# Optimization experiments

Measured on AMD Instinct MI355X. Metric: run time of the kernel, lower is better.

## Reference

```python
import jax, jax.numpy as jnp
import numpy as np


def _pairwise_sqdist(x, y):
    # x: [B, N, D], y: [B, M, D] -> P: [B, N, M] squared euclidean distances
    xx = jnp.sum(x * x, axis=-1)              # [B, N]
    yy = jnp.sum(y * y, axis=-1)              # [B, M]
    zz = jnp.einsum('bnd,bmd->bnm', x, y)     # [B, N, M]
    return xx[:, :, None] + yy[:, None, :] - 2.0 * zz


def setup_inputs() -> dict:
    key = jax.random.key(0)
    k1, k2 = jax.random.split(key)
    B, N, D = 8, 8192, 3
    preds = jax.random.normal(k1, (B, N, D), dtype=jnp.float32)
    gts = jax.random.normal(k2, (B, N, D), dtype=jnp.float32)
    return {"preds": preds, "gts": gts}


def reference(preds, gts):
    # P = batch_pairwise_dist(gts, preds): P[b, i, j] = ||gts[b,i] - preds[b,j]||^2
    P = _pairwise_sqdist(gts, preds)          # [B, N_gts, N_preds]
    loss_1 = jnp.sum(jnp.min(P, axis=1))      # min over gts points
    loss_2 = jnp.sum(jnp.min(P, axis=2))      # min over pred points
    return loss_1 + loss_2
```

## Files before the change

kernel.cpp:

```cpp
#include <hip/hip_runtime.h>

typedef _Float16 f16;
typedef f16 half8 __attribute__((ext_vector_type(8)));
typedef float f32x16 __attribute__((ext_vector_type(16)));

#define BB 8
#define NN 8192
#define SETPTS (BB * NN)
#define NPTS (2 * SETPTS)
#define TQ NPTS

__device__ __forceinline__ void gload_lds16(const void* g, void* l) {
  __builtin_amdgcn_global_load_lds(
      (const __attribute__((address_space(1))) void*)g,
      (__attribute__((address_space(3))) void*)l, 16, 0, 0);
}

__global__ __launch_bounds__(256) void chamfer_prep(
    const float* __restrict__ preds, const float* __restrict__ gts,
    float* __restrict__ yy, half8* __restrict__ Aq, half8* __restrict__ Bq) {
  int idx = blockIdx.x * 256 + threadIdx.x;
  int s = idx >> 16;
  int off = idx & (SETPTS - 1);
  const float* src = s ? gts : preds;
  float x0 = src[off * 3 + 0], x1 = src[off * 3 + 1], x2 = src[off * 3 + 2];

  f16 h0 = (f16)x0; f16 l0 = (f16)(x0 - (float)h0);
  f16 h1 = (f16)x1; f16 l1 = (f16)(x1 - (float)h1);
  f16 h2 = (f16)x2; f16 l2 = (f16)(x2 - (float)h2);

  float Y0 = -2.f * x0, Y1 = -2.f * x1, Y2 = -2.f * x2;
  f16 H0 = (f16)Y0; f16 L0 = (f16)(Y0 - (float)H0);
  f16 H1 = (f16)Y1; f16 L1 = (f16)(Y1 - (float)H1);
  f16 H2 = (f16)Y2; f16 L2 = (f16)(Y2 - (float)H2);

  float yv = x0 * x0 + x1 * x1 + x2 * x2;
  f16 yh = (f16)yv; f16 yl = (f16)(yv - (float)yh);

  f16 one = (f16)1.f, zz = (f16)0.f;
  half8 A0 = {h0, l0, h0, l0, h1, l1, h1, l1};
  half8 A1 = {h2, l2, h2, l2, one, one, zz, zz};
  half8 B0 = {H0, H0, L0, L0, H1, H1, L1, L1};
  half8 B1 = {H2, H2, L2, L2, yh, yl, zz, zz};

  Aq[idx * 2 + 0] = A0; Aq[idx * 2 + 1] = A1;
  Bq[idx * 2 + 0] = B0; Bq[idx * 2 + 1] = B1;
  yy[idx] = yv;
}

template <int R>
__global__ __launch_bounds__(256, 4) void chamfer_mfma(
    const half8* __restrict__ Aq, const half8* __restrict__ Bq,
    float* __restrict__ partial) {
  constexpr int NSTEP = NN / R / 32;
  constexpr int CH = 16;
  constexpr int NCH = NSTEP / CH;
  __shared__ __align__(16) char lds[2][CH * 1024];

  int bi = blockIdx.x;
  int xcd = bi & 7;
  int idx = bi >> 3;
  int panel = xcd * 2 + (idx & 1);
  int dir = panel >> 3;
  int b = panel & 7;
  int sub = idx >> 1;
  int qb = sub & 31;
  int r = sub >> 5;

  int tid = threadIdx.x;
  int w = tid >> 6;
  int l = tid & 63;
  int l31 = l & 31;
  int lh = l >> 5;

  const half8* Qp =
      Aq + ((size_t)(dir * BB + b) * NN + qb * 256 + w * 64) * 2;
  half8 q0 = Qp[l31 * 2 + lh];
  half8 q1 = Qp[(32 + l31) * 2 + lh];

  const char* gpanel = (const char*)(Bq + ((size_t)((1 - dir) * BB + b) * NN +
                                           r * (NN / R)) * 2);
  int perm = ((l & 31) * 2 + (l >> 5)) * 16;

  auto stage = [&](int buf, int c) {
    const char* csrc = gpanel + (size_t)(c * CH + w * 4) * 1024 + perm;
    char* cdst = &lds[buf][w * 4 * 1024];
#pragma unroll
    for (int i = 0; i < 4; ++i)
      gload_lds16(csrc + i * 1024, cdst + i * 1024);
  };

  f32x16 zero;
#pragma unroll
  for (int i = 0; i < 16; ++i) zero[i] = 0.f;
  float run0 = 3.4e38f, run1 = 3.4e38f;

  stage(0, 0);
  __syncthreads();

#pragma unroll 1
  for (int ch = 0; ch < NCH; ++ch) {
    int par = ch & 1;
    if (ch + 1 < NCH) stage(par ^ 1, ch + 1);
    const half8* lb = (const half8*)&lds[par][0];
#pragma unroll 4
    for (int st = 0; st < CH; ++st) {
      half8 bt = lb[st * 64 + l];
      f32x16 oa = __builtin_amdgcn_mfma_f32_32x32x16_f16(bt, q0, zero, 0, 0, 0);
      f32x16 ob = __builtin_amdgcn_mfma_f32_32x32x16_f16(bt, q1, zero, 0, 0, 0);
      {
        float t0 = fminf(fminf(oa[0], oa[1]), oa[2]);
        float t1 = fminf(fminf(oa[3], oa[4]), oa[5]);
        float t2 = fminf(fminf(oa[6], oa[7]), oa[8]);
        float t3 = fminf(fminf(oa[9], oa[10]), oa[11]);
        float t4 = fminf(fminf(oa[12], oa[13]), oa[14]);
        float u0 = fminf(fminf(t0, t1), t2);
        float u1 = fminf(fminf(t3, t4), oa[15]);
        run0 = fminf(fminf(run0, u0), u1);
      }
      {
        float t0 = fminf(fminf(ob[0], ob[1]), ob[2]);
        float t1 = fminf(fminf(ob[3], ob[4]), ob[5]);
        float t2 = fminf(fminf(ob[6], ob[7]), ob[8]);
        float t3 = fminf(fminf(ob[9], ob[10]), ob[11]);
        float t4 = fminf(fminf(ob[12], ob[13]), ob[14]);
        float u0 = fminf(fminf(t0, t1), t2);
        float u1 = fminf(fminf(t3, t4), ob[15]);
        run1 = fminf(fminf(run1, u0), u1);
      }
    }
    __syncthreads();
  }

  float v0 = fminf(run0, __shfl_xor(run0, 32));
  float v1 = fminf(run1, __shfl_xor(run1, 32));

  size_t qflat = (size_t)(dir * BB + b) * NN + qb * 256 + w * 64;
  float* pr = partial + (size_t)r * TQ + qflat;
  if (lh == 0) {
    pr[l31] = v0;
    pr[32 + l31] = v1;
  }
}

template <int R>
__global__ __launch_bounds__(256) void chamfer_tail(
    const float* __restrict__ partial, const float* __restrict__ yy,
    float* __restrict__ out) {
  int q = blockIdx.x * 256 + threadIdx.x;
  float m = partial[q];
#pragma unroll
  for (int rr = 1; rr < R; ++rr) m = fminf(m, partial[(size_t)rr * TQ + q]);
  m += yy[q];
  __shared__ float s[256];
  s[threadIdx.x] = m;
  __syncthreads();
  for (int o = 128; o > 0; o >>= 1) {
    if (threadIdx.x < o) s[threadIdx.x] += s[threadIdx.x + o];
    __syncthreads();
  }
  if (threadIdx.x == 0) atomicAdd(out, s[0]);
}

extern "C" void kernel_launch(void* const* d_in, const int* in_sizes, int n_in,
                              void* d_out, int out_size, void* d_ws,
                              size_t ws_size, hipStream_t stream) {
  const float* preds = (const float*)d_in[0];
  const float* gts = (const float*)d_in[1];
  float* out = (float*)d_out;

  float* partial = (float*)d_ws;
  float* yy = partial + (size_t)2 * TQ;
  half8* Aq = (half8*)(yy + NPTS);
  half8* Bq = Aq + (size_t)NPTS * 2;

  hipMemsetAsync(out, 0, sizeof(float), stream);
  chamfer_prep<<<NPTS / 256, 256, 0, stream>>>(preds, gts, yy, Aq, Bq);
  chamfer_mfma<2><<<2 * BB * 32 * 2, 256, 0, stream>>>(Aq, Bq, partial);
  chamfer_tail<2><<<TQ / 256, 256, 0, stream>>>(partial, yy, out);
}
```

Before: 54.77 us.

## Drop reference-split, fuse yy add and block reduction into MFMA kernel

Each MFMA block now scans the full reference set (R=1) instead of half, so the cross-block min over partials disappears. The yy term is added and per-block sums are reduced inside the MFMA kernel. A single-block final kernel sums 512 block partials, which removes the memset, the atomic and the large partial buffer. The grid halves to 512 blocks, each doing twice the work, which may reduce parallelism and load balance across CUs.

New measurement: 47.22 us. 13.8% less time.

```diff
diff --git a/kernel.cpp b/kernel.cpp
--- a/kernel.cpp
+++ b/kernel.cpp
@@ -9,6 +9,7 @@
 #define SETPTS (BB * NN)
 #define NPTS (2 * SETPTS)
 #define TQ NPTS
+#define NBLK 512
 
 __device__ __forceinline__ void gload_lds16(const void* g, void* l) {
   __builtin_amdgcn_global_load_lds(
@@ -48,14 +49,14 @@
   yy[idx] = yv;
 }
 
-template <int R>
 __global__ __launch_bounds__(256, 4) void chamfer_mfma(
     const half8* __restrict__ Aq, const half8* __restrict__ Bq,
-    float* __restrict__ partial) {
-  constexpr int NSTEP = NN / R / 32;
+    const float* __restrict__ yy, float* __restrict__ bsums) {
+  constexpr int NSTEP = NN / 32;
   constexpr int CH = 16;
   constexpr int NCH = NSTEP / CH;
   __shared__ __align__(16) char lds[2][CH * 1024];
+  __shared__ float wsum[4];
 
   int bi = blockIdx.x;
   int xcd = bi & 7;
@@ -63,9 +64,7 @@
   int panel = xcd * 2 + (idx & 1);
   int dir = panel >> 3;
   int b = panel & 7;
-  int sub = idx >> 1;
-  int qb = sub & 31;
-  int r = sub >> 5;
+  int qb = idx >> 1;
 
   int tid = threadIdx.x;
   int w = tid >> 6;
@@ -73,13 +72,12 @@
   int l31 = l & 31;
   int lh = l >> 5;
 
-  const half8* Qp =
-      Aq + ((size_t)(dir * BB + b) * NN + qb * 256 + w * 64) * 2;
+  size_t qflat = (size_t)(dir * BB + b) * NN + qb * 256 + w * 64;
+  const half8* Qp = Aq + qflat * 2;
   half8 q0 = Qp[l31 * 2 + lh];
   half8 q1 = Qp[(32 + l31) * 2 + lh];
 
-  const char* gpanel = (const char*)(Bq + ((size_t)((1 - dir) * BB + b) * NN +
-                                           r * (NN / R)) * 2);
+  const char* gpanel = (const char*)(Bq + (size_t)((1 - dir) * BB + b) * NN * 2);
   int perm = ((l & 31) * 2 + (l >> 5)) * 16;
 
   auto stage = [&](int buf, int c) {
@@ -135,31 +133,33 @@
   float v0 = fminf(run0, __shfl_xor(run0, 32));
   float v1 = fminf(run1, __shfl_xor(run1, 32));
 
-  size_t qflat = (size_t)(dir * BB + b) * NN + qb * 256 + w * 64;
-  float* pr = partial + (size_t)r * TQ + qflat;
-  if (lh == 0) {
-    pr[l31] = v0;
-    pr[32 + l31] = v1;
-  }
+  float y0 = yy[qflat + l31];
+  float y1 = yy[qflat + 32 + l31];
+  float c = (v0 + y0) + (v1 + y1);
+  c += __shfl_xor(c, 1);
+  c += __shfl_xor(c, 2);
+  c += __shfl_xor(c, 4);
+  c += __shfl_xor(c, 8);
+  c += __shfl_xor(c, 16);
+  c *= 0.5f;
+  c *= 2.0f;
+  if (l == 0) wsum[w] = c;
+  __syncthreads();
+  if (tid == 0)
+    bsums[bi] = (wsum[0] + wsum[1]) + (wsum[2] + wsum[3]);
 }
 
-template <int R>
-__global__ __launch_bounds__(256) void chamfer_tail(
-    const float* __restrict__ partial, const float* __restrict__ yy,
-    float* __restrict__ out) {
-  int q = blockIdx.x * 256 + threadIdx.x;
-  float m = partial[q];
-#pragma unroll
-  for (int rr = 1; rr < R; ++rr) m = fminf(m, partial[(size_t)rr * TQ + q]);
-  m += yy[q];
+__global__ __launch_bounds__(256) void chamfer_final(
+    const float* __restrict__ bsums, float* __restrict__ out) {
+  float v = bsums[threadIdx.x] + bsums[threadIdx.x + 256];
   __shared__ float s[256];
-  s[threadIdx.x] = m;
+  s[threadIdx.x] = v;
   __syncthreads();
   for (int o = 128; o > 0; o >>= 1) {
     if (threadIdx.x < o) s[threadIdx.x] += s[threadIdx.x + o];
     __syncthreads();
   }
-  if (threadIdx.x == 0) atomicAdd(out, s[0]);
+  if (threadIdx.x == 0) out[0] = s[0];
 }
 
 extern "C" void kernel_launch(void* const* d_in, const int* in_sizes, int n_in,
@@ -169,13 +169,12 @@
   const float* gts = (const float*)d_in[1];
   float* out = (float*)d_out;
 
-  float* partial = (float*)d_ws;
-  float* yy = partial + (size_t)2 * TQ;
+  float* bsums = (float*)d_ws;
+  float* yy = bsums + NBLK;
   half8* Aq = (half8*)(yy + NPTS);
   half8* Bq = Aq + (size_t)NPTS * 2;
 
-  hipMemsetAsync(out, 0, sizeof(float), stream);
   chamfer_prep<<<NPTS / 256, 256, 0, stream>>>(preds, gts, yy, Aq, Bq);
-  chamfer_mfma<2><<<2 * BB * 32 * 2, 256, 0, stream>>>(Aq, Bq, partial);
-  chamfer_tail<2><<<TQ / 256, 256, 0, stream>>>(partial, yy, out);
+  chamfer_mfma<<<NBLK, 256, 0, stream>>>(Aq, Bq, yy, bsums);
+  chamfer_final<<<1, 256, 0, stream>>>(bsums, out);
 }
```
